# Optimization experiments

Measured on AMD Instinct MI355X. Metric: run time of the kernel, lower is better.

## Reference

```python
import jax, jax.numpy as jnp
import numpy as np
from jax import lax

WINDOW_SIZE = 11
SIGMA = 1.5
RGB_RANGE = 1.0
K1, K2 = 0.01, 0.03
CHANNELS = 3


def gaussian_window(window_size, sigma, channels, dtype=jnp.float32):
    coords = jnp.arange(window_size, dtype=dtype) - window_size // 2
    g = jnp.exp(-(coords ** 2) / (2.0 * sigma * sigma))
    g = g / g.sum()
    w2d = jnp.outer(g, g)
    w2d = w2d / w2d.sum()
    # depthwise kernel: (C, 1, ws, ws) in OIHW with feature_group_count=C
    return jnp.broadcast_to(w2d, (channels, 1, window_size, window_size)).astype(dtype)


def _dwconv(inp, window, padding):
    # depthwise conv2d, groups = C
    C = inp.shape[1]
    return lax.conv_general_dilated(
        inp, window,
        window_strides=(1, 1),
        padding=[(padding, padding), (padding, padding)],
        feature_group_count=C,
        dimension_numbers=('NCHW', 'OIHW', 'NCHW'))


def setup_inputs() -> dict:
    key = jax.random.key(0)
    kx, ky = jax.random.split(key)
    B, C, H, W = 16, CHANNELS, 512, 512
    x = jax.random.uniform(kx, (B, C, H, W), dtype=jnp.float32)
    y = jax.random.uniform(ky, (B, C, H, W), dtype=jnp.float32)
    window = gaussian_window(WINDOW_SIZE, SIGMA, C)
    return {"x": x, "y": y, "window": window}


def reference(x, y, window):
    padding = WINDOW_SIZE // 2
    mu_x = _dwconv(x, window, padding)
    mu_y = _dwconv(y, window, padding)
    mu_x2 = mu_x * mu_x
    mu_y2 = mu_y * mu_y
    mu_xy = mu_x * mu_y
    sigma_x2 = _dwconv(x * x, window, padding) - mu_x2
    sigma_y2 = _dwconv(y * y, window, padding) - mu_y2
    sigma_xy = _dwconv(x * y, window, padding) - mu_xy
    L = RGB_RANGE
    C1 = (K1 * L) ** 2
    C2 = (K2 * L) ** 2
    ssim_map = ((2.0 * mu_xy + C1) * (2.0 * sigma_xy + C2)) / (
        (mu_x2 + mu_y2 + C1) * (sigma_x2 + sigma_y2 + C2) + 1e-12)
    loss = 1.0 - ssim_map
    return loss.mean()
```

## Files before the change

### kernel.cpp

```cpp
#include <hip/hip_runtime.h>


typedef _Float16 h2 __attribute__((ext_vector_type(2)));
typedef __fp16 fp16x2 __attribute__((ext_vector_type(2)));

__device__ __forceinline__ unsigned h2u(h2 v) { return __builtin_bit_cast(unsigned, v); }
__device__ __forceinline__ unsigned h2u(fp16x2 v) { return __builtin_bit_cast(unsigned, v); }
__device__ __forceinline__ h2 u2h(unsigned u) { return __builtin_bit_cast(h2, u); }
__device__ __forceinline__ h2 pkfma(h2 a, h2 b, h2 c) {
    return __builtin_elementwise_fma(a, b, c);
}
__device__ __forceinline__ unsigned pk2(float a, float b) {
    return h2u(__builtin_amdgcn_cvt_pkrtz(a, b));
}
__device__ __forceinline__ float fdot2_(h2 a, h2 b, float c) {
#if defined(__has_builtin) && __has_builtin(__builtin_amdgcn_fdot2)
    return __builtin_amdgcn_fdot2(a, b, c, false);
#else
    return fmaf((float)a[1], (float)b[1], fmaf((float)a[0], (float)b[0], c));
#endif
}

#define SXW 44
#define HPW 36

__global__ __launch_bounds__(256, 4) void ssim_main(
    const float* __restrict__ xg, const float* __restrict__ yg,
    const float* __restrict__ w2d, float* __restrict__ part)
{
    __shared__ __align__(16) unsigned sxrp[37 * SXW];
    __shared__ __align__(16) unsigned syrp[37 * SXW];
    __shared__ __align__(16) unsigned hq[5][37 * HPW];
    __shared__ float gsf[11];
    __shared__ float wred[4];

    const int tid = threadIdx.x;

    if (tid < 11) {
        float s = 0.0f;
        #pragma unroll
        for (int j = 0; j < 11; ++j) s += w2d[tid * 11 + j];
        gsf[tid] = s;
    }

    const int x0 = blockIdx.x * 32 - 5;
    const int y0 = blockIdx.y * 64 - 5;
    const size_t zoff = (size_t)blockIdx.z * (512 * 512);
    const float* __restrict__ xp = xg + zoff;
    const float* __restrict__ yp = yg + zoff;

    const bool interior = (x0 >= 0) & (x0 + 41 < 512) & (y0 >= 0) & (y0 + 73 < 512);
    if (interior) {
        for (int it = tid; it < 37 * 42; it += 256) {
            const int rp = it / 42, c = it - rp * 42;
            const int o = (y0 + 2 * rp) * 512 + x0 + c;
            sxrp[rp * SXW + c] = pk2(xp[o], xp[o + 512]);
            syrp[rp * SXW + c] = pk2(yp[o], yp[o + 512]);
        }
    } else {
        for (int it = tid; it < 37 * 42; it += 256) {
            const int rp = it / 42, c = it - rp * 42;
            const int gc = x0 + c;
            const int gr0 = y0 + 2 * rp;
            const bool cok = (unsigned)gc < 512u;
            float xv0 = 0.f, xv1 = 0.f, yv0 = 0.f, yv1 = 0.f;
            if (cok && (unsigned)gr0 < 512u) {
                const int o = gr0 * 512 + gc; xv0 = xp[o]; yv0 = yp[o];
            }
            if (cok && (unsigned)(gr0 + 1) < 512u) {
                const int o = (gr0 + 1) * 512 + gc; xv1 = xp[o]; yv1 = yp[o];
            }
            sxrp[rp * SXW + c] = pk2(xv0, xv1);
            syrp[rp * SXW + c] = pk2(yv0, yv1);
        }
    }
    __syncthreads();

    h2 g2[11], ge[6], go[6];
    {
        _Float16 gh[12]; float ssum = 0.0f;
        #pragma unroll
        for (int k = 0; k < 11; ++k) {
            gh[k] = (_Float16)gsf[k];
            if (k != 5) ssum += (float)gh[k];
        }
        gh[5] = (_Float16)(1.0f - ssum);
        gh[11] = (_Float16)0.0f;
        #pragma unroll
        for (int k = 0; k < 11; ++k) g2[k] = (h2){gh[k], gh[k]};
        #pragma unroll
        for (int t = 0; t < 6; ++t) {
            ge[t] = (h2){gh[2 * t], gh[2 * t + 1]};
            go[t] = (h2){(t == 0) ? (_Float16)0.f : gh[2 * t - 1],
                         gh[2 * t]};
        }
    }

    for (int it = tid; it < 37 * 8; it += 256) {
        const int rp = it >> 3, cq = it & 7;
        const int base = rp * SXW + 4 * cq;
        unsigned X[16], Y[16];
        *(uint4*)&X[0]  = *(const uint4*)&sxrp[base];
        *(uint4*)&X[4]  = *(const uint4*)&sxrp[base + 4];
        *(uint4*)&X[8]  = *(const uint4*)&sxrp[base + 8];
        *(uint4*)&X[12] = *(const uint4*)&sxrp[base + 12];
        *(uint4*)&Y[0]  = *(const uint4*)&syrp[base];
        *(uint4*)&Y[4]  = *(const uint4*)&syrp[base + 4];
        *(uint4*)&Y[8]  = *(const uint4*)&syrp[base + 8];
        *(uint4*)&Y[12] = *(const uint4*)&syrp[base + 12];

        const int ob = rp * HPW + 4 * cq;
        auto conv_store = [&](const unsigned* S, int qi) {
            h2 a0 = (h2)0, a1 = (h2)0, a2 = (h2)0, a3 = (h2)0;
            #pragma unroll
            for (int k = 0; k < 11; ++k) {
                const h2 gk = g2[k];
                a0 = pkfma(gk, u2h(S[k]),     a0);
                a1 = pkfma(gk, u2h(S[k + 1]), a1);
                a2 = pkfma(gk, u2h(S[k + 2]), a2);
                a3 = pkfma(gk, u2h(S[k + 3]), a3);
            }
            *(uint4*)&hq[qi][ob] = make_uint4(h2u(a0), h2u(a1), h2u(a2), h2u(a3));
        };

        conv_store(X, 0);
        conv_store(Y, 1);
        unsigned T[14];
        #pragma unroll
        for (int i = 0; i < 14; ++i) { const h2 v = u2h(X[i]); T[i] = h2u(v * v); }
        conv_store(T, 2);
        #pragma unroll
        for (int i = 0; i < 14; ++i) { const h2 v = u2h(Y[i]); T[i] = h2u(v * v); }
        conv_store(T, 3);
        #pragma unroll
        for (int i = 0; i < 14; ++i) { T[i] = h2u(u2h(X[i]) * u2h(Y[i])); }
        conv_store(T, 4);
    }
    __syncthreads();

    const int rq = tid >> 4, cp = tid & 15;
    float A_[5][4][2];
    #pragma unroll
    for (int q = 0; q < 5; ++q)
        #pragma unroll
        for (int e = 0; e < 4; ++e) { A_[q][e][0] = 0.f; A_[q][e][1] = 0.f; }

    #pragma unroll
    for (int q = 0; q < 5; ++q) {
        #pragma unroll
        for (int t = 0; t < 7; ++t) {
            const uint2 V = *(const uint2*)&hq[q][(2 * rq + t) * HPW + 2 * cp];
            const h2 p0 = u2h(V.x), p1 = u2h(V.y);
            if (t < 6) {
                A_[q][0][0] = fdot2_(ge[t], p0, A_[q][0][0]);
                A_[q][0][1] = fdot2_(ge[t], p1, A_[q][0][1]);
                A_[q][1][0] = fdot2_(go[t], p0, A_[q][1][0]);
                A_[q][1][1] = fdot2_(go[t], p1, A_[q][1][1]);
            }
            if (t >= 1) {
                A_[q][2][0] = fdot2_(ge[t - 1], p0, A_[q][2][0]);
                A_[q][2][1] = fdot2_(ge[t - 1], p1, A_[q][2][1]);
                A_[q][3][0] = fdot2_(go[t - 1], p0, A_[q][3][0]);
                A_[q][3][1] = fdot2_(go[t - 1], p1, A_[q][3][1]);
            }
        }
    }

    float lsum = 0.0f;
    const float C1 = 1e-4f, C2 = 9e-4f;
    #pragma unroll
    for (int e = 0; e < 4; ++e) {
        #pragma unroll
        for (int el = 0; el < 2; ++el) {
            const float mx  = A_[0][e][el], my  = A_[1][e][el];
            const float exx = A_[2][e][el], eyy = A_[3][e][el];
            const float exy = A_[4][e][el];
            const float mx2 = mx * mx, my2 = my * my, mxy = mx * my;
            const float vx = exx - mx2, vy = eyy - my2, vxy = exy - mxy;
            const float num = (2.0f * mxy + C1) * (2.0f * vxy + C2);
            const float den = (mx2 + my2 + C1) * (vx + vy + C2) + 1e-12f;
            lsum = fmaf(num, __builtin_amdgcn_rcpf(den), lsum);
        }
    }

    #pragma unroll
    for (int off = 32; off > 0; off >>= 1)
        lsum += __shfl_down(lsum, off, 64);
    if ((tid & 63) == 0) wred[tid >> 6] = lsum;
    __syncthreads();
    if (tid == 0) {
        const int bid = (blockIdx.z * gridDim.y + blockIdx.y) * gridDim.x
                        + blockIdx.x;
        part[bid] = wred[0] + wred[1] + wred[2] + wred[3];
    }
}

__global__ __launch_bounds__(256) void ssim_reduce(
    const float* __restrict__ part, float* __restrict__ out,
    int n, float invN)
{
    __shared__ float wred[4];
    float s = 0.0f;
    for (int i = threadIdx.x; i < n; i += 256) s += part[i];
    #pragma unroll
    for (int off = 32; off > 0; off >>= 1)
        s += __shfl_down(s, off, 64);
    if ((threadIdx.x & 63) == 0) wred[threadIdx.x >> 6] = s;
    __syncthreads();
    if (threadIdx.x == 0)
        out[0] = 1.0f - (wred[0] + wred[1] + wred[2] + wred[3]) * invN;
}

extern "C" void kernel_launch(void* const* d_in, const int* in_sizes, int n_in,
                              void* d_out, int out_size, void* d_ws, size_t ws_size,
                              hipStream_t stream) {
    const float* x   = (const float*)d_in[0];
    const float* y   = (const float*)d_in[1];
    const float* w2d = (const float*)d_in[2];
    float* out  = (float*)d_out;
    float* part = (float*)d_ws;

    const int H = 512, W = 512;
    const int total = in_sizes[0];
    const int Z = total / (H * W);

    dim3 grid(W / 32, H / 64, Z);
    const int nblocks = (W / 32) * (H / 64) * Z;
    ssim_main<<<grid, 256, 0, stream>>>(x, y, w2d, part);

    const float invN = 1.0f / (float)total;
    ssim_reduce<<<1, 256, 0, stream>>>(part, out, nblocks, invN);
}
```

Baseline: 170.8 us.

## Compute separable Gaussian passes with MFMA banded-matrix multiplies

Replaces the packed-half FMA horizontal pass and fdot2 vertical pass with 16x16x32 f16 MFMA instructions. Each pass multiplies by a banded Toeplitz matrix of the Gaussian taps. The input tile is now loaded row-wise with float2 vector loads and column pairs packed, instead of row pairs. This offloads the convolution math to matrix cores, at the cost of redundant multiplies by zero in the banded matrices, a new shared-memory layout, and tricky overlapping tile indexing at the edges.

After: 163.1 us. -4.5%, faster.

```diff
diff --git a/kernel.cpp b/kernel.cpp
--- a/kernel.cpp
+++ b/kernel.cpp
@@ -1,180 +1,161 @@
 #include <hip/hip_runtime.h>
 
 
-typedef _Float16 h2 __attribute__((ext_vector_type(2)));
-typedef __fp16 fp16x2 __attribute__((ext_vector_type(2)));
-
-__device__ __forceinline__ unsigned h2u(h2 v) { return __builtin_bit_cast(unsigned, v); }
-__device__ __forceinline__ unsigned h2u(fp16x2 v) { return __builtin_bit_cast(unsigned, v); }
-__device__ __forceinline__ h2 u2h(unsigned u) { return __builtin_bit_cast(h2, u); }
-__device__ __forceinline__ h2 pkfma(h2 a, h2 b, h2 c) {
-    return __builtin_elementwise_fma(a, b, c);
-}
+typedef __fp16 f16x8 __attribute__((ext_vector_type(8)));
+typedef float f32x4 __attribute__((ext_vector_type(4)));
+typedef unsigned u32x2 __attribute__((ext_vector_type(2)));
+typedef unsigned u32x4 __attribute__((ext_vector_type(4)));
+
 __device__ __forceinline__ unsigned pk2(float a, float b) {
-    return h2u(__builtin_amdgcn_cvt_pkrtz(a, b));
-}
-__device__ __forceinline__ float fdot2_(h2 a, h2 b, float c) {
-#if defined(__has_builtin) && __has_builtin(__builtin_amdgcn_fdot2)
-    return __builtin_amdgcn_fdot2(a, b, c, false);
-#else
-    return fmaf((float)a[1], (float)b[1], fmaf((float)a[0], (float)b[0], c));
-#endif
-}
-
-#define SXW 44
-#define HPW 36
+    return __builtin_bit_cast(unsigned, __builtin_amdgcn_cvt_pkrtz(a, b));
+}
+__device__ __forceinline__ f32x4 mfma16(f16x8 a, f16x8 b, f32x4 c) {
+    return __builtin_amdgcn_mfma_f32_16x16x32_f16(a, b, c, 0, 0, 0);
+}
+__device__ __forceinline__ f16x8 ld8(const unsigned* p) {
+    const u32x2 a = *(const u32x2*)p;
+    const u32x2 b = *(const u32x2*)(p + 2);
+    const u32x4 w = {a.x, a.y, b.x, b.y};
+    return __builtin_bit_cast(f16x8, w);
+}
+
+#define SXW 22
+#define HPW 34
 
 __global__ __launch_bounds__(256, 4) void ssim_main(
     const float* __restrict__ xg, const float* __restrict__ yg,
     const float* __restrict__ w2d, float* __restrict__ part)
 {
-    __shared__ __align__(16) unsigned sxrp[37 * SXW];
-    __shared__ __align__(16) unsigned syrp[37 * SXW];
+    __shared__ __align__(16) unsigned sx[74 * SXW];
+    __shared__ __align__(16) unsigned sy[74 * SXW];
     __shared__ __align__(16) unsigned hq[5][37 * HPW];
-    __shared__ float gsf[11];
+    __shared__ float gsf[12];
     __shared__ float wred[4];
 
     const int tid = threadIdx.x;
 
-    if (tid < 11) {
+    if (tid < 12) {
         float s = 0.0f;
-        #pragma unroll
-        for (int j = 0; j < 11; ++j) s += w2d[tid * 11 + j];
+        if (tid < 11) {
+            #pragma unroll
+            for (int j = 0; j < 11; ++j) s += w2d[tid * 11 + j];
+        }
         gsf[tid] = s;
     }
 
-    const int x0 = blockIdx.x * 32 - 5;
+    const int x0 = blockIdx.x * 32 - 6;
     const int y0 = blockIdx.y * 64 - 5;
     const size_t zoff = (size_t)blockIdx.z * (512 * 512);
     const float* __restrict__ xp = xg + zoff;
     const float* __restrict__ yp = yg + zoff;
 
-    const bool interior = (x0 >= 0) & (x0 + 41 < 512) & (y0 >= 0) & (y0 + 73 < 512);
+    const bool interior = (x0 >= 0) & (x0 + 43 < 512) & (y0 >= 0) & (y0 + 73 < 512);
     if (interior) {
-        for (int it = tid; it < 37 * 42; it += 256) {
-            const int rp = it / 42, c = it - rp * 42;
-            const int o = (y0 + 2 * rp) * 512 + x0 + c;
-            sxrp[rp * SXW + c] = pk2(xp[o], xp[o + 512]);
-            syrp[rp * SXW + c] = pk2(yp[o], yp[o + 512]);
+        for (int it = tid; it < 74 * SXW; it += 256) {
+            const int r = it / SXW, cw = it - r * SXW;
+            const int o = (y0 + r) * 512 + x0 + 2 * cw;
+            const float2 vx = *(const float2*)&xp[o];
+            const float2 vy = *(const float2*)&yp[o];
+            sx[it] = pk2(vx.x, vx.y);
+            sy[it] = pk2(vy.x, vy.y);
         }
     } else {
-        for (int it = tid; it < 37 * 42; it += 256) {
-            const int rp = it / 42, c = it - rp * 42;
-            const int gc = x0 + c;
-            const int gr0 = y0 + 2 * rp;
-            const bool cok = (unsigned)gc < 512u;
+        for (int it = tid; it < 74 * SXW; it += 256) {
+            const int r = it / SXW, cw = it - r * SXW;
+            const int gr = y0 + r, gc = x0 + 2 * cw;
             float xv0 = 0.f, xv1 = 0.f, yv0 = 0.f, yv1 = 0.f;
-            if (cok && (unsigned)gr0 < 512u) {
-                const int o = gr0 * 512 + gc; xv0 = xp[o]; yv0 = yp[o];
+            if ((unsigned)gr < 512u) {
+                const int o = gr * 512 + gc;
+                if ((unsigned)gc < 512u)       { xv0 = xp[o];     yv0 = yp[o]; }
+                if ((unsigned)(gc + 1) < 512u) { xv1 = xp[o + 1]; yv1 = yp[o + 1]; }
             }
-            if (cok && (unsigned)(gr0 + 1) < 512u) {
-                const int o = (gr0 + 1) * 512 + gc; xv1 = xp[o]; yv1 = yp[o];
-            }
-            sxrp[rp * SXW + c] = pk2(xv0, xv1);
-            syrp[rp * SXW + c] = pk2(yv0, yv1);
-        }
-    }
-    __syncthreads();
-
-    h2 g2[11], ge[6], go[6];
-    {
-        _Float16 gh[12]; float ssum = 0.0f;
+            sx[it] = pk2(xv0, xv1);
+            sy[it] = pk2(yv0, yv1);
+        }
+    }
+    __syncthreads();
+
+    const int lane = tid & 63, wv = tid >> 6;
+    const int lm = lane & 15, lg = lane >> 4;
+
+    float ssum = 0.0f;
+    #pragma unroll
+    for (int k = 0; k < 11; ++k)
+        if (k != 5) ssum += (float)(__fp16)gsf[k];
+    const __fp16 cc = (__fp16)(1.0f - ssum);
+    auto tap = [&](int t) -> __fp16 {
+        const unsigned u = ((unsigned)t <= 11u) ? (unsigned)t : 11u;
+        const __fp16 hv = (__fp16)gsf[u];
+        return (t == 5) ? cc : hv;
+    };
+
+    f16x8 bt0, bt1, afr;
+    const int dd = (wv == 3) ? -6 : 0;
+    #pragma unroll
+    for (int e = 0; e < 8; ++e) {
+        const int k = 8 * lg + e;
+        bt0[e] = tap(k - lm - 1);
+        bt1[e] = tap(k - lm - 5);
+        afr[e] = tap(k - lm + dd);
+    }
+
+    for (int i = wv; i < 10; i += 4) {
+        const int b = i >> 1, tl = i & 1;
+        const int rb = (b == 4) ? 58 : 16 * b;
+        const int sbase = (rb + lm) * SXW + 6 * tl + 4 * lg;
+        const f16x8 xa = ld8(&sx[sbase]);
+        const f16x8 ya = ld8(&sy[sbase]);
+        const f16x8 bt = tl ? bt1 : bt0;
+        const f32x4 z4 = {0.f, 0.f, 0.f, 0.f};
+        const f32x4 dmx = mfma16(xa, bt, z4);
+        const f32x4 dmy = mfma16(ya, bt, z4);
+        const f32x4 dxx = mfma16(xa * xa, bt, z4);
+        const f32x4 dyy = mfma16(ya * ya, bt, z4);
+        const f32x4 dxy = mfma16(xa * ya, bt, z4);
+        const int rp0 = (rb >> 1) + 2 * lg;
+        const int col = lm + 16 * tl;
+        hq[0][rp0 * HPW + col]       = pk2(dmx[0], dmx[1]);
+        hq[0][(rp0 + 1) * HPW + col] = pk2(dmx[2], dmx[3]);
+        hq[1][rp0 * HPW + col]       = pk2(dmy[0], dmy[1]);
+        hq[1][(rp0 + 1) * HPW + col] = pk2(dmy[2], dmy[3]);
+        hq[2][rp0 * HPW + col]       = pk2(dxx[0], dxx[1]);
+        hq[2][(rp0 + 1) * HPW + col] = pk2(dxx[2], dxx[3]);
+        hq[3][rp0 * HPW + col]       = pk2(dyy[0], dyy[1]);
+        hq[3][(rp0 + 1) * HPW + col] = pk2(dyy[2], dyy[3]);
+        hq[4][rp0 * HPW + col]       = pk2(dxy[0], dxy[1]);
+        hq[4][(rp0 + 1) * HPW + col] = pk2(dxy[2], dxy[3]);
+    }
+    __syncthreads();
+
+    f32x4 acc[2][5];
+    #pragma unroll
+    for (int ch = 0; ch < 2; ++ch)
         #pragma unroll
-        for (int k = 0; k < 11; ++k) {
-            gh[k] = (_Float16)gsf[k];
-            if (k != 5) ssum += (float)gh[k];
-        }
-        gh[5] = (_Float16)(1.0f - ssum);
-        gh[11] = (_Float16)0.0f;
+        for (int q = 0; q < 5; ++q)
+            acc[ch][q] = (f32x4){0.f, 0.f, 0.f, 0.f};
+
+    const int rpb = (wv == 3) ? 21 : 8 * wv;
+    #pragma unroll
+    for (int ch = 0; ch < 2; ++ch) {
+        const int cb = (rpb + 4 * lg) * HPW + lm + 16 * ch;
         #pragma unroll
-        for (int k = 0; k < 11; ++k) g2[k] = (h2){gh[k], gh[k]};
-        #pragma unroll
-        for (int t = 0; t < 6; ++t) {
-            ge[t] = (h2){gh[2 * t], gh[2 * t + 1]};
-            go[t] = (h2){(t == 0) ? (_Float16)0.f : gh[2 * t - 1],
-                         gh[2 * t]};
-        }
-    }
-
-    for (int it = tid; it < 37 * 8; it += 256) {
-        const int rp = it >> 3, cq = it & 7;
-        const int base = rp * SXW + 4 * cq;
-        unsigned X[16], Y[16];
-        *(uint4*)&X[0]  = *(const uint4*)&sxrp[base];
-        *(uint4*)&X[4]  = *(const uint4*)&sxrp[base + 4];
-        *(uint4*)&X[8]  = *(const uint4*)&sxrp[base + 8];
-        *(uint4*)&X[12] = *(const uint4*)&sxrp[base + 12];
-        *(uint4*)&Y[0]  = *(const uint4*)&syrp[base];
-        *(uint4*)&Y[4]  = *(const uint4*)&syrp[base + 4];
-        *(uint4*)&Y[8]  = *(const uint4*)&syrp[base + 8];
-        *(uint4*)&Y[12] = *(const uint4*)&syrp[base + 12];
-
-        const int ob = rp * HPW + 4 * cq;
-        auto conv_store = [&](const unsigned* S, int qi) {
-            h2 a0 = (h2)0, a1 = (h2)0, a2 = (h2)0, a3 = (h2)0;
-            #pragma unroll
-            for (int k = 0; k < 11; ++k) {
-                const h2 gk = g2[k];
-                a0 = pkfma(gk, u2h(S[k]),     a0);
-                a1 = pkfma(gk, u2h(S[k + 1]), a1);
-                a2 = pkfma(gk, u2h(S[k + 2]), a2);
-                a3 = pkfma(gk, u2h(S[k + 3]), a3);
-            }
-            *(uint4*)&hq[qi][ob] = make_uint4(h2u(a0), h2u(a1), h2u(a2), h2u(a3));
-        };
-
-        conv_store(X, 0);
-        conv_store(Y, 1);
-        unsigned T[14];
-        #pragma unroll
-        for (int i = 0; i < 14; ++i) { const h2 v = u2h(X[i]); T[i] = h2u(v * v); }
-        conv_store(T, 2);
-        #pragma unroll
-        for (int i = 0; i < 14; ++i) { const h2 v = u2h(Y[i]); T[i] = h2u(v * v); }
-        conv_store(T, 3);
-        #pragma unroll
-        for (int i = 0; i < 14; ++i) { T[i] = h2u(u2h(X[i]) * u2h(Y[i])); }
-        conv_store(T, 4);
-    }
-    __syncthreads();
-
-    const int rq = tid >> 4, cp = tid & 15;
-    float A_[5][4][2];
-    #pragma unroll
-    for (int q = 0; q < 5; ++q)
-        #pragma unroll
-        for (int e = 0; e < 4; ++e) { A_[q][e][0] = 0.f; A_[q][e][1] = 0.f; }
-
-    #pragma unroll
-    for (int q = 0; q < 5; ++q) {
-        #pragma unroll
-        for (int t = 0; t < 7; ++t) {
-            const uint2 V = *(const uint2*)&hq[q][(2 * rq + t) * HPW + 2 * cp];
-            const h2 p0 = u2h(V.x), p1 = u2h(V.y);
-            if (t < 6) {
-                A_[q][0][0] = fdot2_(ge[t], p0, A_[q][0][0]);
-                A_[q][0][1] = fdot2_(ge[t], p1, A_[q][0][1]);
-                A_[q][1][0] = fdot2_(go[t], p0, A_[q][1][0]);
-                A_[q][1][1] = fdot2_(go[t], p1, A_[q][1][1]);
-            }
-            if (t >= 1) {
-                A_[q][2][0] = fdot2_(ge[t - 1], p0, A_[q][2][0]);
-                A_[q][2][1] = fdot2_(ge[t - 1], p1, A_[q][2][1]);
-                A_[q][3][0] = fdot2_(go[t - 1], p0, A_[q][3][0]);
-                A_[q][3][1] = fdot2_(go[t - 1], p1, A_[q][3][1]);
-            }
+        for (int q = 0; q < 5; ++q) {
+            const unsigned* hp = hq[q];
+            const u32x4 w4 = {hp[cb], hp[cb + HPW],
+                              hp[cb + 2 * HPW], hp[cb + 3 * HPW]};
+            acc[ch][q] = mfma16(afr, __builtin_bit_cast(f16x8, w4), acc[ch][q]);
         }
     }
 
     float lsum = 0.0f;
     const float C1 = 1e-4f, C2 = 9e-4f;
     #pragma unroll
-    for (int e = 0; e < 4; ++e) {
+    for (int ch = 0; ch < 2; ++ch) {
         #pragma unroll
-        for (int el = 0; el < 2; ++el) {
-            const float mx  = A_[0][e][el], my  = A_[1][e][el];
-            const float exx = A_[2][e][el], eyy = A_[3][e][el];
-            const float exy = A_[4][e][el];
+        for (int r = 0; r < 4; ++r) {
+            const float mx = acc[ch][0][r], my = acc[ch][1][r];
+            const float exx = acc[ch][2][r], eyy = acc[ch][3][r];
+            const float exy = acc[ch][4][r];
             const float mx2 = mx * mx, my2 = my * my, mxy = mx * my;
             const float vx = exx - mx2, vy = eyy - my2, vxy = exy - mxy;
             const float num = (2.0f * mxy + C1) * (2.0f * vxy + C2);
```
